# Optimization experiments

Hardware: AMD Instinct MI355X
Metric: run time of the kernel (lower is better)

The kernel has to match this reference:

```python
import jax, jax.numpy as jnp
import numpy as np

N = 100000   # nodes
E = 800000   # edges (avg degree 8)
IN_DIM = 384
HID = 256
BN_EPS = 1e-5


def setup_inputs() -> dict:
    key = jax.random.key(0)
    ks = jax.random.split(key, 12)
    x = jax.random.normal(ks[0], (N, IN_DIM), dtype=jnp.float32)
    edge_index = jax.random.randint(ks[1], (2, E), 0, N, dtype=jnp.int32)
    # GCNConv params (glorot-ish scaling)
    W1 = jax.random.normal(ks[2], (IN_DIM, HID), dtype=jnp.float32) * (1.0 / np.sqrt(IN_DIM))
    b1 = jnp.zeros((HID,), jnp.float32)
    W2 = jax.random.normal(ks[3], (HID, HID), dtype=jnp.float32) * (1.0 / np.sqrt(HID))
    b2 = jnp.zeros((HID,), jnp.float32)
    # BatchNorm affine params
    g1 = jnp.ones((HID,), jnp.float32)
    be1 = jnp.zeros((HID,), jnp.float32)
    g2 = jnp.ones((HID,), jnp.float32)
    be2 = jnp.zeros((HID,), jnp.float32)
    return {"x": x, "edge_index": edge_index, "W1": W1, "b1": b1, "g1": g1,
            "be1": be1, "W2": W2, "b2": b2, "g2": g2, "be2": be2}


def _gcn_conv(x, W, b, src, dst):
    """PyG GCNConv: self-loops + symmetric normalization D^-1/2 A D^-1/2."""
    h = x @ W                                             # [N, H]
    deg = jnp.zeros((x.shape[0],), h.dtype).at[dst].add(1.0) + 1.0  # in-deg + self loop
    dinv = jax.lax.rsqrt(deg)                             # [N]
    coef = dinv[src] * dinv[dst]                          # [E]
    agg = jnp.zeros_like(h).at[dst].add(h[src] * coef[:, None])     # scatter-add messages
    agg = agg + h * (1.0 / deg)[:, None]                  # self-loop term (norm = 1/deg)
    return agg + b


def _batchnorm(h, gamma, beta):
    # training-mode BN over node dim, biased variance (matches torch normalization)
    mu = jnp.mean(h, axis=0)
    var = jnp.mean(jnp.square(h - mu), axis=0)
    return gamma * (h - mu) * jax.lax.rsqrt(var + BN_EPS) + beta


def reference(x, edge_index, W1, b1, g1, be1, W2, b2, g2, be2):
    src, dst = edge_index[0], edge_index[1]
    h = _gcn_conv(x, W1, b1, src, dst)
    h = jax.nn.relu(_batchnorm(h, g1, be1))
    # dropout: eval mode -> identity
    h = _gcn_conv(h, W2, b2, src, dst)
    h = jax.nn.relu(_batchnorm(h, g2, be2))
    return h
```

## Files before the change

kernel.cpp:

```cpp
#include <hip/hip_runtime.h>
#include <hip/hip_bf16.h>

#define NN  100000
#define NE  800000
#define KIN 384
#define HID 256
#define BN_EPS 1e-5f

typedef __attribute__((ext_vector_type(4))) float floatx4;
typedef __attribute__((ext_vector_type(8))) short short8;

__device__ __forceinline__ unsigned short f2b(float f) {
    union { float f; unsigned int u; } v; v.f = f;
    unsigned int r = v.u + 0x7fffu + ((v.u >> 16) & 1u);
    return (unsigned short)(r >> 16);
}
__device__ __forceinline__ float b2f(unsigned short h) {
    union { unsigned int u; float f; } v; v.u = ((unsigned int)h) << 16;
    return v.f;
}

__global__ void k_wt2(const float* __restrict__ W1, unsigned short* __restrict__ W1t,
                      const float* __restrict__ W2, unsigned short* __restrict__ W2t) {
    const int n = threadIdx.x;
    const int k = blockIdx.x;
    if (k < KIN) W1t[(size_t)n * KIN + k] = f2b(W1[(size_t)k * HID + n]);
    else {
        const int k2 = k - KIN;
        W2t[(size_t)n * HID + k2] = f2b(W2[(size_t)k2 * HID + n]);
    }
}

__global__ void k_count(const int* __restrict__ dst, int* __restrict__ deg) {
    int i = blockIdx.x * 256 + threadIdx.x;
    if (i < NE) atomicAdd(deg + dst[i], 1);
}

__device__ __forceinline__ int block_incl_scan(int v, int* lds) {
    lds[threadIdx.x] = v; __syncthreads();
    #pragma unroll
    for (int off = 1; off < 256; off <<= 1) {
        int t = lds[threadIdx.x];
        int a = (threadIdx.x >= off) ? lds[threadIdx.x - off] : 0;
        __syncthreads();
        lds[threadIdx.x] = t + a;
        __syncthreads();
    }
    return lds[threadIdx.x];
}

__global__ __launch_bounds__(256) void k_scan1(const int* __restrict__ deg,
                                               int* __restrict__ bsum,
                                               float* __restrict__ dinv) {
    __shared__ int lds[256];
    int i = blockIdx.x * 256 + threadIdx.x;
    int v = (i < NN) ? deg[i] : 0;
    if (i < NN) dinv[i] = rsqrtf((float)(v + 1));
    int incl = block_incl_scan(v, lds);
    if (threadIdx.x == 255) bsum[blockIdx.x] = incl;
}

__global__ __launch_bounds__(512) void k_scan2(const int* __restrict__ bsum,
                                               int* __restrict__ boff, int nb,
                                               int* __restrict__ rowptr) {
    __shared__ int lds[512];
    int v = (threadIdx.x < nb) ? bsum[threadIdx.x] : 0;
    lds[threadIdx.x] = v; __syncthreads();
    #pragma unroll
    for (int off = 1; off < 512; off <<= 1) {
        int t = lds[threadIdx.x];
        int a = (threadIdx.x >= off) ? lds[threadIdx.x - off] : 0;
        __syncthreads();
        lds[threadIdx.x] = t + a;
        __syncthreads();
    }
    if (threadIdx.x < nb) boff[threadIdx.x] = lds[threadIdx.x] - v;
    if (threadIdx.x == 0) rowptr[NN] = NE;
}

__global__ __launch_bounds__(256) void k_scan3(const int* __restrict__ deg,
                                               const int* __restrict__ boff,
                                               int* __restrict__ rowptr) {
    __shared__ int lds[256];
    int i = blockIdx.x * 256 + threadIdx.x;
    int v = (i < NN) ? deg[i] : 0;
    int incl = block_incl_scan(v, lds);
    if (i < NN) rowptr[i] = incl - v + boff[blockIdx.x];
}

__global__ __launch_bounds__(256) void k_fill(
    const int* __restrict__ src, const int* __restrict__ dst,
    const float* __restrict__ dinv, const int* __restrict__ rowptr,
    int* __restrict__ cursor, int2* __restrict__ epk)
{
    int e = blockIdx.x * 256 + threadIdx.x;
    if (e < NE) {
        const int d = dst[e], s = src[e];
        const int pos = rowptr[d] + atomicAdd(cursor + d, 1);
        int2 rec; rec.x = s; rec.y = __float_as_int(dinv[s]);
        epk[pos] = rec;
    }
}

template<int K, int MODE, int ABF16>
__global__ __launch_bounds__(512) void k_gemm(
    const void* __restrict__ Av, const unsigned short* __restrict__ Bt,
    unsigned short* __restrict__ C,
    const float* __restrict__ scale, const float* __restrict__ bias, int M)
{
    constexpr int BM = 128, BK = 32, LD = 40;
    __shared__ __align__(16) unsigned short As[BM * LD];
    __shared__ __align__(16) unsigned short Bs[HID * LD];
    const int tid = threadIdx.x;
    const int lane = tid & 63;
    const int wid  = tid >> 6;
    const int wm = wid & 1, wn = wid >> 1;
    const int l15 = lane & 15, lq = lane >> 4;
    const int row0 = blockIdx.x * BM;

    floatx4 acc[4][4] = {};

    const int ar  = tid >> 3;
    const int ak  = (tid & 7) * 4;
    const int ar2 = tid >> 2;
    const int ak2 = (tid & 3) * 8;
    const int bn_ = tid >> 2;
    const int bk  = (tid & 3) * 8;

    for (int k0 = 0; k0 < K; k0 += BK) {
        if (ABF16) {
            const unsigned short* A = (const unsigned short*)Av;
            const int grow = row0 + ar2;
            float x[8];
            if (grow < M) {
                short8 v = *(const short8*)(A + (size_t)grow * K + k0 + ak2);
                #pragma unroll
                for (int t = 0; t < 8; ++t) x[t] = b2f((unsigned short)v[t]);
                if (MODE) {
                    float4 s0 = *(const float4*)(scale + k0 + ak2);
                    float4 s1 = *(const float4*)(scale + k0 + ak2 + 4);
                    float4 b0 = *(const float4*)(bias  + k0 + ak2);
                    float4 b1 = *(const float4*)(bias  + k0 + ak2 + 4);
                    x[0] = fmaxf(x[0] * s0.x + b0.x, 0.f);
                    x[1] = fmaxf(x[1] * s0.y + b0.y, 0.f);
                    x[2] = fmaxf(x[2] * s0.z + b0.z, 0.f);
                    x[3] = fmaxf(x[3] * s0.w + b0.w, 0.f);
                    x[4] = fmaxf(x[4] * s1.x + b1.x, 0.f);
                    x[5] = fmaxf(x[5] * s1.y + b1.y, 0.f);
                    x[6] = fmaxf(x[6] * s1.z + b1.z, 0.f);
                    x[7] = fmaxf(x[7] * s1.w + b1.w, 0.f);
                }
            } else {
                #pragma unroll
                for (int t = 0; t < 8; ++t) x[t] = 0.f;
            }
            short8 o;
            #pragma unroll
            for (int t = 0; t < 8; ++t) o[t] = (short)f2b(x[t]);
            *(short8*)(As + ar2 * LD + ak2) = o;
        } else {
            const float* A = (const float*)Av;
            #pragma unroll
            for (int p = 0; p < 2; ++p) {
                const int row  = p * 64 + ar;
                const int grow = row0 + row;
                float x0 = 0.f, x1 = 0.f, x2 = 0.f, x3 = 0.f;
                if (grow < M) {
                    float4 v = *(const float4*)(A + (size_t)grow * K + k0 + ak);
                    x0 = v.x; x1 = v.y; x2 = v.z; x3 = v.w;
                }
                ushort4 o;
                o.x = f2b(x0); o.y = f2b(x1); o.z = f2b(x2); o.w = f2b(x3);
                *(ushort4*)(As + row * LD + ak) = o;
            }
        }
        #pragma unroll
        for (int p = 0; p < 2; ++p) {
            const int n = p * 128 + bn_;
            *(float4*)(Bs + n * LD + bk) =
                *(const float4*)(Bt + (size_t)n * K + k0 + bk);
        }
        __syncthreads();

        short8 af[4], bf[4];
        #pragma unroll
        for (int i = 0; i < 4; ++i)
            af[i] = *(const short8*)(As + (wm * 64 + i * 16 + l15) * LD + lq * 8);
        #pragma unroll
        for (int j = 0; j < 4; ++j)
            bf[j] = *(const short8*)(Bs + (wn * 64 + j * 16 + l15) * LD + lq * 8);
        #pragma unroll
        for (int i = 0; i < 4; ++i)
            #pragma unroll
            for (int j = 0; j < 4; ++j)
                acc[i][j] = __builtin_amdgcn_mfma_f32_16x16x32_bf16(af[i], bf[j], acc[i][j], 0, 0, 0);
        __syncthreads();
    }

    #pragma unroll
    for (int i = 0; i < 4; ++i) {
        #pragma unroll
        for (int r = 0; r < 4; ++r) {
            const int m = row0 + wm * 64 + i * 16 + lq * 4 + r;
            if (m < M) {
                #pragma unroll
                for (int j = 0; j < 4; ++j) {
                    const int c = wn * 64 + j * 16 + l15;
                    C[(size_t)m * HID + c] = f2b(acc[i][j][r]);
                }
            }
        }
    }
}

__global__ __launch_bounds__(256) void k_gather(
    const unsigned short* __restrict__ H, const int2* __restrict__ epk,
    const int* __restrict__ rowptr, const float* __restrict__ dinv,
    unsigned short* __restrict__ AGGb, float* __restrict__ bn_acc)
{
    __shared__ float ls[512];
    const int tid = threadIdx.x, lane = tid & 63, w = tid >> 6;
    const int c0 = lane * 4;
    float sx = 0.f, sy = 0.f, sz = 0.f, sw = 0.f;
    float qx = 0.f, qy = 0.f, qz = 0.f, qw = 0.f;

    for (int n = blockIdx.x * 4 + w; n < NN; n += gridDim.x * 4) {
        const int beg = rowptr[n], end = rowptr[n + 1];
        const float di = dinv[n];
        float ax = 0.f, ay = 0.f, az = 0.f, aw = 0.f;
        int j = beg;
        for (; j + 4 <= end; j += 4) {
            const int2 e0 = epk[j], e1 = epk[j + 1], e2 = epk[j + 2], e3 = epk[j + 3];
            const ushort4 h0 = *(const ushort4*)(H + (size_t)e0.x * HID + c0);
            const ushort4 h1 = *(const ushort4*)(H + (size_t)e1.x * HID + c0);
            const ushort4 h2 = *(const ushort4*)(H + (size_t)e2.x * HID + c0);
            const ushort4 h3 = *(const ushort4*)(H + (size_t)e3.x * HID + c0);
            const float f0 = __int_as_float(e0.y) * di, f1 = __int_as_float(e1.y) * di;
            const float f2 = __int_as_float(e2.y) * di, f3 = __int_as_float(e3.y) * di;
            ax += b2f(h0.x) * f0 + b2f(h1.x) * f1 + b2f(h2.x) * f2 + b2f(h3.x) * f3;
            ay += b2f(h0.y) * f0 + b2f(h1.y) * f1 + b2f(h2.y) * f2 + b2f(h3.y) * f3;
            az += b2f(h0.z) * f0 + b2f(h1.z) * f1 + b2f(h2.z) * f2 + b2f(h3.z) * f3;
            aw += b2f(h0.w) * f0 + b2f(h1.w) * f1 + b2f(h2.w) * f2 + b2f(h3.w) * f3;
        }
        for (; j < end; ++j) {
            const int2 e0 = epk[j];
            const float f0 = __int_as_float(e0.y) * di;
            const ushort4 h0 = *(const ushort4*)(H + (size_t)e0.x * HID + c0);
            ax += b2f(h0.x) * f0; ay += b2f(h0.y) * f0;
            az += b2f(h0.z) * f0; aw += b2f(h0.w) * f0;
        }
        const float cs = di * di;
        const ushort4 hs = *(const ushort4*)(H + (size_t)n * HID + c0);
        ax += b2f(hs.x) * cs; ay += b2f(hs.y) * cs;
        az += b2f(hs.z) * cs; aw += b2f(hs.w) * cs;

        ushort4 o;
        o.x = f2b(ax); o.y = f2b(ay); o.z = f2b(az); o.w = f2b(aw);
        *(ushort4*)(AGGb + (size_t)n * HID + c0) = o;

        sx += ax; sy += ay; sz += az; sw += aw;
        qx += ax * ax; qy += ay * ay; qz += az * az; qw += aw * aw;
    }

    ls[tid] = 0.f; ls[tid + 256] = 0.f;
    __syncthreads();
    atomicAdd(&ls[c0 + 0], sx); atomicAdd(&ls[c0 + 1], sy);
    atomicAdd(&ls[c0 + 2], sz); atomicAdd(&ls[c0 + 3], sw);
    atomicAdd(&ls[256 + c0 + 0], qx); atomicAdd(&ls[256 + c0 + 1], qy);
    atomicAdd(&ls[256 + c0 + 2], qz); atomicAdd(&ls[256 + c0 + 3], qw);
    __syncthreads();
    atomicAdd(bn_acc + tid, ls[tid]);
    atomicAdd(bn_acc + 256 + tid, ls[tid + 256]);
}

__global__ void k_bnparam(const float* __restrict__ bn_acc,
                          const float* __restrict__ g, const float* __restrict__ be,
                          float* __restrict__ scale, float* __restrict__ bias)
{
    const int c = threadIdx.x;
    const float inv_n = 1.f / (float)NN;
    const float mu  = bn_acc[c] * inv_n;
    const float var = bn_acc[256 + c] * inv_n - mu * mu;
    const float sc  = g[c] * rsqrtf(var + BN_EPS);
    scale[c] = sc;
    bias[c]  = be[c] - sc * mu;
}

__global__ __launch_bounds__(256) void k_apply(
    const unsigned short* __restrict__ AGGb, const float* __restrict__ scale,
    const float* __restrict__ bias, float* __restrict__ out)
{
    const int gid = blockIdx.x * 256 + threadIdx.x;
    if (gid < NN * (HID / 4)) {
        const int c4 = (gid & 63) * 4;
        ushort4 v = *(const ushort4*)(AGGb + (size_t)gid * 4);
        float4 sc = *(const float4*)(scale + c4);
        float4 bi = *(const float4*)(bias + c4);
        float4 o;
        o.x = fmaxf(b2f(v.x) * sc.x + bi.x, 0.f);
        o.y = fmaxf(b2f(v.y) * sc.y + bi.y, 0.f);
        o.z = fmaxf(b2f(v.z) * sc.z + bi.z, 0.f);
        o.w = fmaxf(b2f(v.w) * sc.w + bi.w, 0.f);
        *(float4*)(out + (size_t)gid * 4) = o;
    }
}

extern "C" void kernel_launch(void* const* d_in, const int* in_sizes, int n_in,
                              void* d_out, int out_size, void* d_ws, size_t ws_size,
                              hipStream_t stream)
{
    const float* x   = (const float*)d_in[0];
    const int*   ei  = (const int*)d_in[1];
    const float* W1  = (const float*)d_in[2];
    const float* g1  = (const float*)d_in[4];
    const float* be1 = (const float*)d_in[5];
    const float* W2  = (const float*)d_in[6];
    const float* g2  = (const float*)d_in[8];
    const float* be2 = (const float*)d_in[9];
    float* out = (float*)d_out;
    const int* srcp = ei;
    const int* dstp = ei + NE;

    constexpr int NB = (NN + 255) / 256;

    char* p = (char*)d_ws;
    int*            deg    = (int*)p;             p += (size_t)NN * 4;
    int*            cursor = (int*)p;             p += (size_t)NN * 4;
    float*          bn1    = (float*)p;           p += 512 * 4;
    float*          bn2    = (float*)p;           p += 512 * 4;
    const size_t zbytes = (size_t)NN * 8 + 4096;
    unsigned short* AGGb   = (unsigned short*)p;  p += (size_t)NN * HID * 2;
    unsigned short* H      = (unsigned short*)p;  p += (size_t)NN * HID * 2;
    float*          dinv   = (float*)p;           p += (size_t)NN * 4;
    int*            rowptr = (int*)p;             p += (size_t)(NN + 1) * 4;
    int2*           epk    = (int2*)p;            p += (size_t)NE * 8;
    int*            bsum   = (int*)p;             p += 512 * 4;
    int*            boff   = (int*)p;             p += 512 * 4;
    unsigned short* W1t    = (unsigned short*)p;  p += (size_t)KIN * HID * 2;
    unsigned short* W2t    = (unsigned short*)p;  p += (size_t)HID * HID * 2;
    float*          sc1    = (float*)p;           p += 256 * 4;
    float*          bi1    = (float*)p;           p += 256 * 4;
    float*          sc2    = (float*)p;           p += 256 * 4;
    float*          bi2    = (float*)p;           p += 256 * 4;

    hipMemsetAsync(deg, 0, zbytes, stream);

    k_wt2<<<KIN + HID, HID, 0, stream>>>(W1, W1t, W2, W2t);

    k_count<<<(NE + 255) / 256, 256, 0, stream>>>(dstp, deg);
    k_scan1<<<NB, 256, 0, stream>>>(deg, bsum, dinv);
    k_scan2<<<1, 512, 0, stream>>>(bsum, boff, NB, rowptr);
    k_scan3<<<NB, 256, 0, stream>>>(deg, boff, rowptr);
    k_fill<<<(NE + 255) / 256, 256, 0, stream>>>(srcp, dstp, dinv, rowptr, cursor, epk);

    const int ggrid = (NN + 127) / 128;

    k_gemm<KIN, 0, 0><<<ggrid, 512, 0, stream>>>(x, W1t, H, nullptr, nullptr, NN);
    k_gather<<<2048, 256, 0, stream>>>(H, epk, rowptr, dinv, AGGb, bn1);
    k_bnparam<<<1, 256, 0, stream>>>(bn1, g1, be1, sc1, bi1);

    k_gemm<HID, 1, 1><<<ggrid, 512, 0, stream>>>(AGGb, W2t, H, sc1, bi1, NN);
    k_gather<<<2048, 256, 0, stream>>>(H, epk, rowptr, dinv, AGGb, bn2);
    k_bnparam<<<1, 256, 0, stream>>>(bn2, g2, be2, sc2, bi2);
    k_apply<<<(NN * (HID / 4) + 255) / 256, 256, 0, stream>>>(AGGb, sc2, bi2, out);
}
```

Before: 678.1 us.

## Fold BN param kernel into consumers and split gather edges across half-waves

Removes the two single-block k_bnparam launches by computing BN scale and bias inside the GEMM (into shared memory) and inside k_apply (per thread). Rewrites the gather so each half-wave handles alternate edges with 16-byte loads of 8 channels, then combines the halves with a cross-lane shuffle. This doubles the edge-level parallelism per node and widens the loads. The gather also gets an occupancy hint of 6 and a smaller grid. Costs are the redundant BN parameter computation in every k_apply thread and the shuffle reduction.

```diff
diff --git a/kernel.cpp b/kernel.cpp
--- a/kernel.cpp
+++ b/kernel.cpp
@@ -106,17 +106,31 @@
 __global__ __launch_bounds__(512) void k_gemm(
     const void* __restrict__ Av, const unsigned short* __restrict__ Bt,
     unsigned short* __restrict__ C,
-    const float* __restrict__ scale, const float* __restrict__ bias, int M)
+    const float* __restrict__ bnacc, const float* __restrict__ g,
+    const float* __restrict__ be, int M)
 {
     constexpr int BM = 128, BK = 32, LD = 40;
     __shared__ __align__(16) unsigned short As[BM * LD];
     __shared__ __align__(16) unsigned short Bs[HID * LD];
+    __shared__ float s_sc[HID], s_bi[HID];
     const int tid = threadIdx.x;
     const int lane = tid & 63;
     const int wid  = tid >> 6;
     const int wm = wid & 1, wn = wid >> 1;
     const int l15 = lane & 15, lq = lane >> 4;
     const int row0 = blockIdx.x * BM;
+
+    if (MODE) {
+        if (tid < HID) {
+            const float inv_n = 1.f / (float)NN;
+            const float mu  = bnacc[tid] * inv_n;
+            const float var = bnacc[HID + tid] * inv_n - mu * mu;
+            const float s   = g[tid] * rsqrtf(var + BN_EPS);
+            s_sc[tid] = s;
+            s_bi[tid] = be[tid] - s * mu;
+        }
+        __syncthreads();
+    }
 
     floatx4 acc[4][4] = {};
 
@@ -137,10 +151,10 @@
                 #pragma unroll
                 for (int t = 0; t < 8; ++t) x[t] = b2f((unsigned short)v[t]);
                 if (MODE) {
-                    float4 s0 = *(const float4*)(scale + k0 + ak2);
-                    float4 s1 = *(const float4*)(scale + k0 + ak2 + 4);
-                    float4 b0 = *(const float4*)(bias  + k0 + ak2);
-                    float4 b1 = *(const float4*)(bias  + k0 + ak2 + 4);
+                    float4 s0 = *(const float4*)(s_sc + k0 + ak2);
+                    float4 s1 = *(const float4*)(s_sc + k0 + ak2 + 4);
+                    float4 b0 = *(const float4*)(s_bi + k0 + ak2);
+                    float4 b1 = *(const float4*)(s_bi + k0 + ak2 + 4);
                     x[0] = fmaxf(x[0] * s0.x + b0.x, 0.f);
                     x[1] = fmaxf(x[1] * s0.y + b0.y, 0.f);
                     x[2] = fmaxf(x[2] * s0.z + b0.z, 0.f);
@@ -213,94 +227,108 @@
     }
 }
 
-__global__ __launch_bounds__(256) void k_gather(
+__global__ __launch_bounds__(256, 6) void k_gather(
     const unsigned short* __restrict__ H, const int2* __restrict__ epk,
     const int* __restrict__ rowptr, const float* __restrict__ dinv,
     unsigned short* __restrict__ AGGb, float* __restrict__ bn_acc)
 {
     __shared__ float ls[512];
     const int tid = threadIdx.x, lane = tid & 63, w = tid >> 6;
-    const int c0 = lane * 4;
-    float sx = 0.f, sy = 0.f, sz = 0.f, sw = 0.f;
-    float qx = 0.f, qy = 0.f, qz = 0.f, qw = 0.f;
+    const int half = lane >> 5;
+    const int l32  = lane & 31;
+    const int c0   = l32 * 8;
+    float s[8] = {}, q[8] = {};
 
     for (int n = blockIdx.x * 4 + w; n < NN; n += gridDim.x * 4) {
         const int beg = rowptr[n], end = rowptr[n + 1];
         const float di = dinv[n];
-        float ax = 0.f, ay = 0.f, az = 0.f, aw = 0.f;
+        float a[8] = {};
         int j = beg;
-        for (; j + 4 <= end; j += 4) {
-            const int2 e0 = epk[j], e1 = epk[j + 1], e2 = epk[j + 2], e3 = epk[j + 3];
-            const ushort4 h0 = *(const ushort4*)(H + (size_t)e0.x * HID + c0);
-            const ushort4 h1 = *(const ushort4*)(H + (size_t)e1.x * HID + c0);
-            const ushort4 h2 = *(const ushort4*)(H + (size_t)e2.x * HID + c0);
-            const ushort4 h3 = *(const ushort4*)(H + (size_t)e3.x * HID + c0);
-            const float f0 = __int_as_float(e0.y) * di, f1 = __int_as_float(e1.y) * di;
-            const float f2 = __int_as_float(e2.y) * di, f3 = __int_as_float(e3.y) * di;
-            ax += b2f(h0.x) * f0 + b2f(h1.x) * f1 + b2f(h2.x) * f2 + b2f(h3.x) * f3;
-            ay += b2f(h0.y) * f0 + b2f(h1.y) * f1 + b2f(h2.y) * f2 + b2f(h3.y) * f3;
-            az += b2f(h0.z) * f0 + b2f(h1.z) * f1 + b2f(h2.z) * f2 + b2f(h3.z) * f3;
-            aw += b2f(h0.w) * f0 + b2f(h1.w) * f1 + b2f(h2.w) * f2 + b2f(h3.w) * f3;
-        }
-        for (; j < end; ++j) {
-            const int2 e0 = epk[j];
-            const float f0 = __int_as_float(e0.y) * di;
-            const ushort4 h0 = *(const ushort4*)(H + (size_t)e0.x * HID + c0);
-            ax += b2f(h0.x) * f0; ay += b2f(h0.y) * f0;
-            az += b2f(h0.z) * f0; aw += b2f(h0.w) * f0;
-        }
-        const float cs = di * di;
-        const ushort4 hs = *(const ushort4*)(H + (size_t)n * HID + c0);
-        ax += b2f(hs.x) * cs; ay += b2f(hs.y) * cs;
-        az += b2f(hs.z) * cs; aw += b2f(hs.w) * cs;
-
-        ushort4 o;
-        o.x = f2b(ax); o.y = f2b(ay); o.z = f2b(az); o.w = f2b(aw);
-        *(ushort4*)(AGGb + (size_t)n * HID + c0) = o;
-
-        sx += ax; sy += ay; sz += az; sw += aw;
-        qx += ax * ax; qy += ay * ay; qz += az * az; qw += aw * aw;
+        for (; j + 8 <= end; j += 8) {
+            #pragma unroll
+            for (int t = 0; t < 4; ++t) {
+                const int2 e = epk[j + half + 2 * t];
+                const float cf = __int_as_float(e.y) * di;
+                const short8 h = *(const short8*)(H + (size_t)e.x * HID + c0);
+                #pragma unroll
+                for (int u = 0; u < 8; ++u)
+                    a[u] += b2f((unsigned short)h[u]) * cf;
+            }
+        }
+        for (; j + 2 <= end; j += 2) {
+            const int2 e = epk[j + half];
+            const float cf = __int_as_float(e.y) * di;
+            const short8 h = *(const short8*)(H + (size_t)e.x * HID + c0);
+            #pragma unroll
+            for (int u = 0; u < 8; ++u)
+                a[u] += b2f((unsigned short)h[u]) * cf;
+        }
+        if (j < end && half == 0) {
+            const int2 e = epk[j];
+            const float cf = __int_as_float(e.y) * di;
+            const short8 h = *(const short8*)(H + (size_t)e.x * HID + c0);
+            #pragma unroll
+            for (int u = 0; u < 8; ++u)
+                a[u] += b2f((unsigned short)h[u]) * cf;
+        }
+        if (half == 1) {
+            const float cs = di * di;
+            const short8 h = *(const short8*)(H + (size_t)n * HID + c0);
+            #pragma unroll
+            for (int u = 0; u < 8; ++u)
+                a[u] += b2f((unsigned short)h[u]) * cs;
+        }
+        #pragma unroll
+        for (int u = 0; u < 8; ++u)
+            a[u] += __shfl_xor(a[u], 32);
+        if (half == 0) {
+            short8 o;
+            #pragma unroll
+            for (int u = 0; u < 8; ++u) o[u] = (short)f2b(a[u]);
+            *(short8*)(AGGb + (size_t)n * HID + c0) = o;
+            #pragma unroll
+            for (int u = 0; u < 8; ++u) { s[u] += a[u]; q[u] += a[u] * a[u]; }
+        }
     }
 
     ls[tid] = 0.f; ls[tid + 256] = 0.f;
     __syncthreads();
-    atomicAdd(&ls[c0 + 0], sx); atomicAdd(&ls[c0 + 1], sy);
-    atomicAdd(&ls[c0 + 2], sz); atomicAdd(&ls[c0 + 3], sw);
-    atomicAdd(&ls[256 + c0 + 0], qx); atomicAdd(&ls[256 + c0 + 1], qy);
-    atomicAdd(&ls[256 + c0 + 2], qz); atomicAdd(&ls[256 + c0 + 3], qw);
+    if (half == 0) {
+        #pragma unroll
+        for (int u = 0; u < 8; ++u) {
+            atomicAdd(&ls[c0 + u], s[u]);
+            atomicAdd(&ls[256 + c0 + u], q[u]);
+        }
+    }
     __syncthreads();
     atomicAdd(bn_acc + tid, ls[tid]);
     atomicAdd(bn_acc + 256 + tid, ls[tid + 256]);
 }
 
-__global__ void k_bnparam(const float* __restrict__ bn_acc,
-                          const float* __restrict__ g, const float* __restrict__ be,
-                          float* __restrict__ scale, float* __restrict__ bias)
-{
-    const int c = threadIdx.x;
-    const float inv_n = 1.f / (float)NN;
-    const float mu  = bn_acc[c] * inv_n;
-    const float var = bn_acc[256 + c] * inv_n - mu * mu;
-    const float sc  = g[c] * rsqrtf(var + BN_EPS);
-    scale[c] = sc;
-    bias[c]  = be[c] - sc * mu;
-}
-
 __global__ __launch_bounds__(256) void k_apply(
-    const unsigned short* __restrict__ AGGb, const float* __restrict__ scale,
-    const float* __restrict__ bias, float* __restrict__ out)
+    const unsigned short* __restrict__ AGGb, const float* __restrict__ bnacc,
+    const float* __restrict__ g, const float* __restrict__ be,
+    float* __restrict__ out)
 {
     const int gid = blockIdx.x * 256 + threadIdx.x;
     if (gid < NN * (HID / 4)) {
         const int c4 = (gid & 63) * 4;
+        float sc[4], bi[4];
+        const float inv_n = 1.f / (float)NN;
+        #pragma unroll
+        for (int u = 0; u < 4; ++u) {
+            const int c = c4 + u;
+            const float mu  = bnacc[c] * inv_n;
+            const float var = bnacc[HID + c] * inv_n - mu * mu;
+            const float sv  = g[c] * rsqrtf(var + BN_EPS);
+            sc[u] = sv; bi[u] = be[c] - sv * mu;
+        }
         ushort4 v = *(const ushort4*)(AGGb + (size_t)gid * 4);
-        float4 sc = *(const float4*)(scale + c4);
-        float4 bi = *(const float4*)(bias + c4);
         float4 o;
-        o.x = fmaxf(b2f(v.x) * sc.x + bi.x, 0.f);
-        o.y = fmaxf(b2f(v.y) * sc.y + bi.y, 0.f);
-        o.z = fmaxf(b2f(v.z) * sc.z + bi.z, 0.f);
-        o.w = fmaxf(b2f(v.w) * sc.w + bi.w, 0.f);
+        o.x = fmaxf(b2f(v.x) * sc[0] + bi[0], 0.f);
+        o.y = fmaxf(b2f(v.y) * sc[1] + bi[1], 0.f);
+        o.z = fmaxf(b2f(v.z) * sc[2] + bi[2], 0.f);
+        o.w = fmaxf(b2f(v.w) * sc[3] + bi[3], 0.f);
         *(float4*)(out + (size_t)gid * 4) = o;
     }
 }
@@ -338,10 +366,6 @@
     int*            boff   = (int*)p;             p += 512 * 4;
     unsigned short* W1t    = (unsigned short*)p;  p += (size_t)KIN * HID * 2;
     unsigned short* W2t    = (unsigned short*)p;  p += (size_t)HID * HID * 2;
-    float*          sc1    = (float*)p;           p += 256 * 4;
-    float*          bi1    = (float*)p;           p += 256 * 4;
-    float*          sc2    = (float*)p;           p += 256 * 4;
-    float*          bi2    = (float*)p;           p += 256 * 4;
 
     hipMemsetAsync(deg, 0, zbytes, stream);
 
@@ -355,12 +379,10 @@
 
     const int ggrid = (NN + 127) / 128;
 
-    k_gemm<KIN, 0, 0><<<ggrid, 512, 0, stream>>>(x, W1t, H, nullptr, nullptr, NN);
-    k_gather<<<2048, 256, 0, stream>>>(H, epk, rowptr, dinv, AGGb, bn1);
-    k_bnparam<<<1, 256, 0, stream>>>(bn1, g1, be1, sc1, bi1);
-
-    k_gemm<HID, 1, 1><<<ggrid, 512, 0, stream>>>(AGGb, W2t, H, sc1, bi1, NN);
-    k_gather<<<2048, 256, 0, stream>>>(H, epk, rowptr, dinv, AGGb, bn2);
-    k_bnparam<<<1, 256, 0, stream>>>(bn2, g2, be2, sc2, bi2);
-    k_apply<<<(NN * (HID / 4) + 255) / 256, 256, 0, stream>>>(AGGb, sc2, bi2, out);
-}
+    k_gemm<KIN, 0, 0><<<ggrid, 512, 0, stream>>>(x, W1t, H, nullptr, nullptr, nullptr, NN);
+    k_gather<<<1536, 256, 0, stream>>>(H, epk, rowptr, dinv, AGGb, bn1);
+
+    k_gemm<HID, 1, 1><<<ggrid, 512, 0, stream>>>(AGGb, W2t, H, bn1, g1, be1, NN);
+    k_gather<<<1536, 256, 0, stream>>>(H, epk, rowptr, dinv, AGGb, bn2);
+    k_apply<<<(NN * (HID / 4) + 255) / 256, 256, 0, stream>>>(AGGb, bn2, g2, be2, out);
+}
```

After: 661.1 us. 1.03x faster.
